# Optimization experiments

Measured on AMD Instinct MI355X. Metric: run time of the kernel, lower is better.

Reference implementation:

```python
import jax, jax.numpy as jnp
import numpy as np

B = 64        # graphs per batch
NP = 96       # nodes per graph
H = 64        # hid_size
IN_F = 32     # node feature dim
E_F = 16      # edge feature dim
DEG = 8       # avg degree
ENSEMBLE = 1


def _lin(key, fan_in, fan_out):
    return jax.random.normal(key, (fan_in, fan_out), jnp.float32) / np.float32(np.sqrt(fan_in))


def setup_inputs() -> dict:
    key = jax.random.key(0)
    ks = jax.random.split(key, 12)
    N = B * NP
    E = B * NP * DEG
    x = jax.random.normal(ks[0], (N, IN_F), jnp.float32)
    edge_attr = jax.random.normal(ks[1], (E, E_F), jnp.float32)
    # within-graph random edges (sorted per-graph blocks, like is_sorted=True)
    rng = np.random.default_rng(0)
    off = (np.arange(B) * NP)[:, None]
    src = (rng.integers(0, NP, size=(B, NP * DEG)) + off).ravel()
    dst = (rng.integers(0, NP, size=(B, NP * DEG)) + off).ravel()
    edge_index = jnp.asarray(np.stack([src, dst]), dtype=jnp.int32)
    # idx = concat of triu_indices(n, -n) per graph == ALL n^2 pairs per graph
    tri = np.triu_indices(NP, -NP)
    idx0 = jnp.asarray((tri[0][None, :] + off).ravel(), jnp.int32)  # [B*NP^2]
    idx1 = jnp.asarray((tri[1][None, :] + off).ravel(), jnp.int32)
    params = dict(
        W_atom=_lin(ks[2], IN_F, H), b_atom=jnp.zeros((H,), jnp.float32),
        W_bond=_lin(ks[3], E_F, H), b_bond=jnp.zeros((H,), jnp.float32),
        W_node=_lin(ks[4], H, H), b_node=jnp.zeros((H,), jnp.float32),
        W_edge=_lin(ks[5], H, H), b_edge=jnp.zeros((H,), jnp.float32),
        W1=_lin(ks[6], 3 * H, H), b1=jnp.zeros((H,), jnp.float32),
        W2=_lin(ks[7], H, H), b2=jnp.zeros((H,), jnp.float32),
        W3=_lin(ks[8], H, ENSEMBLE), b3=jnp.zeros((ENSEMBLE,), jnp.float32),
    )
    return dict(x=x, edge_attr=edge_attr, edge_index=edge_index,
                idx0=idx0, idx1=idx1, n=NP, **params)


def reference(x, edge_attr, edge_index, idx0, idx1, n,
              W_atom, b_atom, W_bond, b_bond, W_node, b_node,
              W_edge, b_edge, W1, b1, W2, b2, W3, b3):
    # encoders
    xh = x @ W_atom + b_atom                 # [N, H]
    eh = edge_attr @ W_bond + b_bond         # [E, H]
    emb_n = xh @ W_node + b_node             # [N, H]
    emb_e = eh @ W_edge + b_edge             # [E, H]
    # SparseTensor.to_dense() then gather at idx == scatter-add edge embeddings
    # into the per-graph dense pairwise slot (duplicates sum, missing = 0),
    # without materializing the O(N^2) adjacency.
    u, v = edge_index[0], edge_index[1]
    g = u // n
    pair_idx = g * (n * n) + (u - g * n) * n + (v - g * n)   # [E]
    P = idx0.shape[0]                         # B * n^2, idx enumerates all pairs row-major
    pair_e = jnp.zeros((P, emb_e.shape[1]), emb_e.dtype).at[pair_idx].add(emb_e)
    emb = jnp.concatenate((emb_n[idx0], emb_n[idx1], pair_e), axis=-1)  # [P, 3H]
    # MLP [3H, H, H, ensemble], plain last layer
    h = jax.nn.relu(emb @ W1 + b1)
    h = jax.nn.relu(h @ W2 + b2)
    return h @ W3 + b3                        # [P, ensemble]
```

## Files before the change

kernel.cpp:

```cpp
#include <hip/hip_runtime.h>

#define NPG 96
#define BGR 64
#define HID 64
#define INF 32
#define EF  16
#define DEG 8
#define NN  (BGR*NPG)
#define NE  (BGR*NPG*DEG)
#define EPG (NPG*DEG)
#define PPG (NPG*NPG)

typedef short bf16x8 __attribute__((ext_vector_type(8)));
typedef float f32x4  __attribute__((ext_vector_type(4)));

__device__ __forceinline__ unsigned rne2(float lo, float hi) {
    union { float f; unsigned u; } a, b; a.f = lo; b.f = hi;
    unsigned ua = a.u + 0x7FFF + ((a.u >> 16) & 1);
    unsigned ub = b.u + 0x7FFF + ((b.u >> 16) & 1);
    return (ua >> 16) | (ub & 0xFFFF0000u);
}
__device__ __forceinline__ unsigned short rne1(float x) {
    union { float f; unsigned u; } a; a.f = x;
    return (unsigned short)((a.u + 0x7FFF + ((a.u >> 16) & 1)) >> 16);
}

__global__ __launch_bounds__(256) void node_kernel(
    const float* __restrict__ x,
    const float* __restrict__ W_atom, const float* __restrict__ b_atom,
    const float* __restrict__ W_node, const float* __restrict__ b_node,
    const float* __restrict__ W1,     const float* __restrict__ b1,
    float* __restrict__ Abuf, float* __restrict__ Bbuf)
{
    __shared__ float sh[4][64];
    const int wave = threadIdx.x >> 6, lane = threadIdx.x & 63;
    const int n = __builtin_amdgcn_readfirstlane(blockIdx.x * 4 + wave);
    const float* xr = x + n * INF;

    float xh = b_atom[lane];
    #pragma unroll
    for (int k = 0; k < INF; ++k) xh += xr[k] * W_atom[k*HID + lane];
    sh[wave][lane] = xh;
    __syncthreads();

    float en = b_node[lane];
    #pragma unroll
    for (int k = 0; k < HID; ++k) en += sh[wave][k] * W_node[k*HID + lane];
    __syncthreads();
    sh[wave][lane] = en;
    __syncthreads();

    float a = b1[lane], b = 0.f;
    #pragma unroll
    for (int k = 0; k < HID; ++k) {
        const float ek = sh[wave][k];
        a += ek * W1[k*HID + lane];
        b += ek * W1[(HID + k)*HID + lane];
    }
    Abuf[n*HID + lane] = a;
    Bbuf[n*HID + lane] = b;
}

#define SBST 68
#define W2ST 72
__global__ __launch_bounds__(256) void pair_dense_kernel(
    const float* __restrict__ Abuf, const float* __restrict__ Bbuf,
    const float* __restrict__ W2,   const float* __restrict__ b2,
    const float* __restrict__ W3,   const float* __restrict__ b3,
    float* __restrict__ out)
{
    __shared__ float sB[NPG * SBST];
    __shared__ float sA[8 * 64];
    __shared__ unsigned short sW2t[64 * W2ST];
    const int t  = threadIdx.x;
    const int g  = blockIdx.x / 12;
    const int i0 = (blockIdx.x % 12) * 8;

    const float* Bg = Bbuf + g * NPG * 64;
    for (int idx = t; idx < NPG*64; idx += 256)
        sB[(idx >> 6)*SBST + (idx & 63)] = Bg[idx];
    for (int idx = t; idx < 8*64; idx += 256)
        sA[idx] = Abuf[(g*NPG + i0 + (idx >> 6))*64 + (idx & 63)];
    for (int idx = t; idx < 64*64; idx += 256) {
        const int k = idx >> 6, n = idx & 63;
        sW2t[n*W2ST + k] = rne1(W2[idx]);
    }
    __syncthreads();

    const int wave = t >> 6, lane = t & 63;
    const int col = lane & 15, q = lane >> 4;

    bf16x8 w2f[4][2];
    #pragma unroll
    for (int nt = 0; nt < 4; ++nt)
        #pragma unroll
        for (int c = 0; c < 2; ++c)
            w2f[nt][c] = *(const bf16x8*)(sW2t + (nt*16 + col)*W2ST + c*32 + q*8);

    float w3l[4], b2l[4];
    #pragma unroll
    for (int nt = 0; nt < 4; ++nt) {
        w3l[nt] = W3[nt*16 + col];
        b2l[nt] = b2[nt*16 + col];
    }
    const float b3v = b3[0];

    #pragma unroll
    for (int ii = 0; ii < 2; ++ii) {
        const int il = wave*2 + ii;
        float areg[16];
        {
            const float4* Ar = (const float4*)(sA + il*64 + q*8);
            const float4 a0 = Ar[0], a1 = Ar[1];
            const float4 a2 = Ar[8], a3 = Ar[9];
            areg[0]=a0.x; areg[1]=a0.y; areg[2]=a0.z; areg[3]=a0.w;
            areg[4]=a1.x; areg[5]=a1.y; areg[6]=a1.z; areg[7]=a1.w;
            areg[8]=a2.x; areg[9]=a2.y; areg[10]=a2.z; areg[11]=a2.w;
            areg[12]=a3.x; areg[13]=a3.y; areg[14]=a3.z; areg[15]=a3.w;
        }
        float* outr = out + g*PPG + (i0 + il)*NPG;

        for (int jc = 0; jc < 6; ++jc) {
            const int j0 = jc * 16;
            union { bf16x8 v; unsigned u[4]; } h1[2];
            const float* Brow = sB + (j0 + col)*SBST + q*8;
            #pragma unroll
            for (int c = 0; c < 2; ++c) {
                const float4 b0 = *(const float4*)(Brow + c*32);
                const float4 b1v = *(const float4*)(Brow + c*32 + 4);
                float h[8];
                h[0] = fmaxf(areg[c*8+0] + b0.x, 0.f);
                h[1] = fmaxf(areg[c*8+1] + b0.y, 0.f);
                h[2] = fmaxf(areg[c*8+2] + b0.z, 0.f);
                h[3] = fmaxf(areg[c*8+3] + b0.w, 0.f);
                h[4] = fmaxf(areg[c*8+4] + b1v.x, 0.f);
                h[5] = fmaxf(areg[c*8+5] + b1v.y, 0.f);
                h[6] = fmaxf(areg[c*8+6] + b1v.z, 0.f);
                h[7] = fmaxf(areg[c*8+7] + b1v.w, 0.f);
                #pragma unroll
                for (int p2 = 0; p2 < 4; ++p2)
                    h1[c].u[p2] = rne2(h[2*p2], h[2*p2+1]);
            }
            f32x4 acc[4];
            #pragma unroll
            for (int nt = 0; nt < 4; ++nt) {
                f32x4 z = {0.f, 0.f, 0.f, 0.f};
                z = __builtin_amdgcn_mfma_f32_16x16x32_bf16(h1[0].v, w2f[nt][0], z, 0, 0, 0);
                z = __builtin_amdgcn_mfma_f32_16x16x32_bf16(h1[1].v, w2f[nt][1], z, 0, 0, 0);
                acc[nt] = z;
            }
            float p[4];
            #pragma unroll
            for (int r = 0; r < 4; ++r) {
                float s = 0.f;
                #pragma unroll
                for (int nt = 0; nt < 4; ++nt)
                    s += fmaxf(acc[nt][r] + b2l[nt], 0.f) * w3l[nt];
                p[r] = s;
            }
            #pragma unroll
            for (int off = 1; off < 16; off <<= 1) {
                #pragma unroll
                for (int r = 0; r < 4; ++r)
                    p[r] += __shfl_xor(p[r], off, 64);
            }
            if (col == 0) {
                float4 o = make_float4(p[0]+b3v, p[1]+b3v, p[2]+b3v, p[3]+b3v);
                *(float4*)(outr + j0 + q*4) = o;
            }
        }
    }
}

__global__ __launch_bounds__(EPG) void dedup_kernel(
    const float* __restrict__ ea,  const int* __restrict__ eidx,
    const float* __restrict__ W_bond, const float* __restrict__ b_bond,
    const float* __restrict__ W_edge, const float* __restrict__ b_edge,
    const float* __restrict__ W1,
    int* __restrict__ fkey, int* __restrict__ fcnt,
    float* __restrict__ fsea, int* __restrict__ gcount,
    float* __restrict__ wec, float* __restrict__ biascg)
{
    __shared__ int   head[PPG];
    __shared__ int   nxt[EPG];
    __shared__ float sU[16*64];
    __shared__ float sbe[64];
    __shared__ int   lcnt;
    const int t = threadIdx.x;
    const int g = blockIdx.x;

    for (int idx = t; idx < PPG; idx += EPG) head[idx] = -1;
    if (t == 0) lcnt = 0;

    const int u = eidx[g*EPG + t]      - g*NPG;
    const int v = eidx[NE + g*EPG + t] - g*NPG;
    const int key = u*NPG + v;
    __syncthreads();

    nxt[t] = atomicExch(&head[key], t);
    __syncthreads();

    if (head[key] == t) {
        const float* eag = ea + (size_t)g * EPG * EF;
        float s[EF];
        #pragma unroll
        for (int q = 0; q < EF; ++q) s[q] = 0.f;
        int cnt = 0;
        for (int e = t; e != -1; e = nxt[e]) {
            ++cnt;
            const float4* p = (const float4*)(eag + e*EF);
            #pragma unroll
            for (int q4 = 0; q4 < 4; ++q4) {
                const float4 f = p[q4];
                s[q4*4+0] += f.x; s[q4*4+1] += f.y;
                s[q4*4+2] += f.z; s[q4*4+3] += f.w;
            }
        }
        const int pos  = atomicAdd(&lcnt, 1);
        const int slot = g*EPG + pos;
        fkey[slot] = key;
        fcnt[slot] = cnt;
        #pragma unroll
        for (int q = 0; q < EF; ++q) fsea[slot*EF + q] = s[q];
    }
    __syncthreads();
    if (t == 0) gcount[g] = lcnt;

    if (g == 0) {
        for (int idx = t; idx < 16*64; idx += EPG) {
            const int r = idx >> 6, c = idx & 63;
            float s = 0.f;
            for (int k = 0; k < 64; ++k) s += W_bond[r*64+k] * W_edge[k*64+c];
            sU[idx] = s;
        }
        if (t < 64) {
            float s2 = b_edge[t];
            for (int k = 0; k < 64; ++k) s2 += b_bond[k] * W_edge[k*64+t];
            sbe[t] = s2;
        }
        __syncthreads();
        for (int idx = t; idx < 16*64; idx += EPG) {
            const int r = idx >> 6, c = idx & 63;
            float s = 0.f;
            for (int k = 0; k < 64; ++k) s += sU[r*64+k] * W1[(128+k)*64+c];
            wec[idx] = s;
        }
        if (t < 64) {
            float sc = 0.f;
            for (int k = 0; k < 64; ++k) sc += sbe[k] * W1[(128+k)*64+t];
            biascg[t] = sc;
        }
    }
}

#define FIXW 16
#define FIX_BLOCKS (NE / (FIXW * 4))
__global__ __launch_bounds__(256) void fixmlp_kernel(
    const float* __restrict__ Abuf, const float* __restrict__ Bbuf,
    const int* __restrict__ fkey, const int* __restrict__ fcnt,
    const float* __restrict__ fsea, const int* __restrict__ gcount,
    const float* __restrict__ wec,  const float* __restrict__ biascg,
    const float* __restrict__ W2,   const float* __restrict__ b2,
    const float* __restrict__ W3,   const float* __restrict__ b3,
    float* __restrict__ out)
{
    __shared__ unsigned short sW2t[64 * W2ST];
    __shared__ float sWEc[16*64];
    __shared__ float sbc[64];
    const int t = threadIdx.x;

    for (int idx = t; idx < 64*64; idx += 256) {
        const int k = idx >> 6, n = idx & 63;
        sW2t[n*W2ST + k] = rne1(W2[idx]);
    }
    for (int idx = t; idx < 16*64; idx += 256) sWEc[idx] = wec[idx];
    if (t < 64) sbc[t] = biascg[t];
    __syncthreads();

    const int wave = t >> 6, lane = t & 63;
    const int col = lane & 15, q = lane >> 4;
    const int s0 = (blockIdx.x * 4 + wave) * FIXW;
    const int g  = s0 / EPG;
    const int l0 = s0 % EPG;
    const int cg = gcount[g];
    if (l0 >= cg) return;

    bf16x8 w2f[4][2];
    #pragma unroll
    for (int nt = 0; nt < 4; ++nt)
        #pragma unroll
        for (int c = 0; c < 2; ++c)
            w2f[nt][c] = *(const bf16x8*)(sW2t + (nt*16 + col)*W2ST + c*32 + q*8);

    float w3l[4], b2l[4];
    #pragma unroll
    for (int nt = 0; nt < 4; ++nt) {
        w3l[nt] = W3[nt*16 + col];
        b2l[nt] = b2[nt*16 + col];
    }
    const float b3v = b3[0];
    const int k0 = q * 8;

    union { bf16x8 v; unsigned u[4]; } h1[2];
    #pragma unroll
    for (int p2 = 0; p2 < 4; ++p2) { h1[0].u[p2] = 0; h1[1].u[p2] = 0; }

    const int s = s0 + col;
    if (l0 + col < cg) {
        const int key  = fkey[s];
        const float cf = (float)fcnt[s];
        const int ui = key / NPG, vi = key % NPG;

        float se[16];
        {
            const float4* p = (const float4*)(fsea + (size_t)s * EF);
            #pragma unroll
            for (int q4 = 0; q4 < 4; ++q4) {
                const float4 f = p[q4];
                se[q4*4+0] = f.x; se[q4*4+1] = f.y;
                se[q4*4+2] = f.z; se[q4*4+3] = f.w;
            }
        }

        float ck[16];
        #pragma unroll
        for (int kk = 0; kk < 8; ++kk) {
            ck[kk]     = cf * sbc[k0 + kk];
            ck[8 + kk] = cf * sbc[32 + k0 + kk];
        }
        #pragma unroll
        for (int qq = 0; qq < 16; ++qq) {
            const float sq = se[qq];
            const float4 w0 = *(const float4*)(sWEc + qq*64 + k0);
            const float4 w1 = *(const float4*)(sWEc + qq*64 + k0 + 4);
            const float4 w2v = *(const float4*)(sWEc + qq*64 + k0 + 32);
            const float4 w3v = *(const float4*)(sWEc + qq*64 + k0 + 36);
            ck[0]  += sq * w0.x;  ck[1]  += sq * w0.y;
            ck[2]  += sq * w0.z;  ck[3]  += sq * w0.w;
            ck[4]  += sq * w1.x;  ck[5]  += sq * w1.y;
            ck[6]  += sq * w1.z;  ck[7]  += sq * w1.w;
            ck[8]  += sq * w2v.x; ck[9]  += sq * w2v.y;
            ck[10] += sq * w2v.z; ck[11] += sq * w2v.w;
            ck[12] += sq * w3v.x; ck[13] += sq * w3v.y;
            ck[14] += sq * w3v.z; ck[15] += sq * w3v.w;
        }

        const float* Ar = Abuf + (g*NPG + ui)*64;
        const float* Br = Bbuf + (g*NPG + vi)*64;
        const float4 a0 = *(const float4*)(Ar + k0);
        const float4 a1 = *(const float4*)(Ar + k0 + 4);
        const float4 a2 = *(const float4*)(Ar + k0 + 32);
        const float4 a3 = *(const float4*)(Ar + k0 + 36);
        const float4 c0 = *(const float4*)(Br + k0);
        const float4 c1 = *(const float4*)(Br + k0 + 4);
        const float4 c2 = *(const float4*)(Br + k0 + 32);
        const float4 c3 = *(const float4*)(Br + k0 + 36);

        float h[16];
        h[0]  = fmaxf(a0.x + c0.x + ck[0],  0.f);
        h[1]  = fmaxf(a0.y + c0.y + ck[1],  0.f);
        h[2]  = fmaxf(a0.z + c0.z + ck[2],  0.f);
        h[3]  = fmaxf(a0.w + c0.w + ck[3],  0.f);
        h[4]  = fmaxf(a1.x + c1.x + ck[4],  0.f);
        h[5]  = fmaxf(a1.y + c1.y + ck[5],  0.f);
        h[6]  = fmaxf(a1.z + c1.z + ck[6],  0.f);
        h[7]  = fmaxf(a1.w + c1.w + ck[7],  0.f);
        h[8]  = fmaxf(a2.x + c2.x + ck[8],  0.f);
        h[9]  = fmaxf(a2.y + c2.y + ck[9],  0.f);
        h[10] = fmaxf(a2.z + c2.z + ck[10], 0.f);
        h[11] = fmaxf(a2.w + c2.w + ck[11], 0.f);
        h[12] = fmaxf(a3.x + c3.x + ck[12], 0.f);
        h[13] = fmaxf(a3.y + c3.y + ck[13], 0.f);
        h[14] = fmaxf(a3.z + c3.z + ck[14], 0.f);
        h[15] = fmaxf(a3.w + c3.w + ck[15], 0.f);
        #pragma unroll
        for (int p2 = 0; p2 < 4; ++p2) {
            h1[0].u[p2] = rne2(h[2*p2],     h[2*p2 + 1]);
            h1[1].u[p2] = rne2(h[8 + 2*p2], h[8 + 2*p2 + 1]);
        }
    }

    f32x4 acc[4];
    #pragma unroll
    for (int nt = 0; nt < 4; ++nt) {
        f32x4 z = {0.f, 0.f, 0.f, 0.f};
        z = __builtin_amdgcn_mfma_f32_16x16x32_bf16(h1[0].v, w2f[nt][0], z, 0, 0, 0);
        z = __builtin_amdgcn_mfma_f32_16x16x32_bf16(h1[1].v, w2f[nt][1], z, 0, 0, 0);
        acc[nt] = z;
    }

    float p[4];
    #pragma unroll
    for (int r = 0; r < 4; ++r) {
        float sum = 0.f;
        #pragma unroll
        for (int nt = 0; nt < 4; ++nt)
            sum += fmaxf(acc[nt][r] + b2l[nt], 0.f) * w3l[nt];
        p[r] = sum;
    }
    #pragma unroll
    for (int off = 1; off < 16; off <<= 1) {
        #pragma unroll
        for (int r = 0; r < 4; ++r)
            p[r] += __shfl_xor(p[r], off, 64);
    }
    if (col == 0) {
        #pragma unroll
        for (int r = 0; r < 4; ++r) {
            const int lr = q*4 + r;
            if (l0 + lr < cg) {
                const int keyr = fkey[s0 + lr];
                out[g*PPG + keyr] = p[r] + b3v;
            }
        }
    }
}

extern "C" void kernel_launch(void* const* d_in, const int* in_sizes, int n_in,
                              void* d_out, int out_size, void* d_ws, size_t ws_size,
                              hipStream_t stream)
{
    const float* x      = (const float*)d_in[0];
    const float* ea     = (const float*)d_in[1];
    const int*   eidx   = (const int*)  d_in[2];
    const float* W_atom = (const float*)d_in[6];
    const float* b_atom = (const float*)d_in[7];
    const float* W_bond = (const float*)d_in[8];
    const float* b_bond = (const float*)d_in[9];
    const float* W_node = (const float*)d_in[10];
    const float* b_node = (const float*)d_in[11];
    const float* W_edge = (const float*)d_in[12];
    const float* b_edge = (const float*)d_in[13];
    const float* W1     = (const float*)d_in[14];
    const float* b1     = (const float*)d_in[15];
    const float* W2     = (const float*)d_in[16];
    const float* b2     = (const float*)d_in[17];
    const float* W3     = (const float*)d_in[18];
    const float* b3     = (const float*)d_in[19];
    float* out = (float*)d_out;

    float* ws    = (float*)d_ws;
    float* Abuf  = ws;
    float* Bbuf  = Abuf  + NN*HID;
    float* fsea  = Bbuf  + NN*HID;
    int*   fkey  = (int*)(fsea + NE*EF);
    int*   fcnt  = fkey + NE;
    int*   gcount= fcnt + NE;
    float* wec   = (float*)(gcount + BGR);
    float* biascg= wec + 16*64;

    node_kernel<<<NN/4, 256, 0, stream>>>(x, W_atom, b_atom, W_node, b_node,
                                          W1, b1, Abuf, Bbuf);
    dedup_kernel<<<BGR, EPG, 0, stream>>>(ea, eidx, W_bond, b_bond,
                                          W_edge, b_edge, W1,
                                          fkey, fcnt, fsea, gcount,
                                          wec, biascg);
    pair_dense_kernel<<<BGR*12, 256, 0, stream>>>(Abuf, Bbuf,
                                                  W2, b2, W3, b3, out);
    fixmlp_kernel<<<FIX_BLOCKS, 256, 0, stream>>>(
        Abuf, Bbuf, fkey, fcnt, fsea, gcount, wec, biascg,
        W2, b2, W3, b3, out);
}
```

Before: 152.9 us.

## Merge four kernels into two and mask dense writes with edge bitmap

The node encoder and edge dedup kernels are fused into one prep launch that uses block-index ranges, with 12 nodes per 768-thread block. The dense pair MLP and edge-fix MLP are fused into one pair launch. A per-graph bitmap of pairs that have edges is built during dedup, and the dense path skips writing outputs for those pairs. This removes two launches and lets both pair paths run concurrently, because the fix path no longer has to overwrite dense results after them. The cost is a larger shared-memory footprint per block and per-element bitmap checks on output stores.

Result: faster. 142.4 us (-6.9%).

```diff
diff --git a/kernel.cpp b/kernel.cpp
--- a/kernel.cpp
+++ b/kernel.cpp
@@ -10,6 +10,7 @@
 #define NE  (BGR*NPG*DEG)
 #define EPG (NPG*DEG)
 #define PPG (NPG*NPG)
+#define BMW 288
 
 typedef short bf16x8 __attribute__((ext_vector_type(8)));
 typedef float f32x4  __attribute__((ext_vector_type(4)));
@@ -25,172 +26,65 @@
     return (unsigned short)((a.u + 0x7FFF + ((a.u >> 16) & 1)) >> 16);
 }
 
-__global__ __launch_bounds__(256) void node_kernel(
+__global__ __launch_bounds__(768) void prep_kernel(
     const float* __restrict__ x,
     const float* __restrict__ W_atom, const float* __restrict__ b_atom,
     const float* __restrict__ W_node, const float* __restrict__ b_node,
     const float* __restrict__ W1,     const float* __restrict__ b1,
-    float* __restrict__ Abuf, float* __restrict__ Bbuf)
-{
-    __shared__ float sh[4][64];
-    const int wave = threadIdx.x >> 6, lane = threadIdx.x & 63;
-    const int n = __builtin_amdgcn_readfirstlane(blockIdx.x * 4 + wave);
-    const float* xr = x + n * INF;
-
-    float xh = b_atom[lane];
-    #pragma unroll
-    for (int k = 0; k < INF; ++k) xh += xr[k] * W_atom[k*HID + lane];
-    sh[wave][lane] = xh;
-    __syncthreads();
-
-    float en = b_node[lane];
-    #pragma unroll
-    for (int k = 0; k < HID; ++k) en += sh[wave][k] * W_node[k*HID + lane];
-    __syncthreads();
-    sh[wave][lane] = en;
-    __syncthreads();
-
-    float a = b1[lane], b = 0.f;
-    #pragma unroll
-    for (int k = 0; k < HID; ++k) {
-        const float ek = sh[wave][k];
-        a += ek * W1[k*HID + lane];
-        b += ek * W1[(HID + k)*HID + lane];
-    }
-    Abuf[n*HID + lane] = a;
-    Bbuf[n*HID + lane] = b;
-}
-
-#define SBST 68
-#define W2ST 72
-__global__ __launch_bounds__(256) void pair_dense_kernel(
-    const float* __restrict__ Abuf, const float* __restrict__ Bbuf,
-    const float* __restrict__ W2,   const float* __restrict__ b2,
-    const float* __restrict__ W3,   const float* __restrict__ b3,
-    float* __restrict__ out)
-{
-    __shared__ float sB[NPG * SBST];
-    __shared__ float sA[8 * 64];
-    __shared__ unsigned short sW2t[64 * W2ST];
-    const int t  = threadIdx.x;
-    const int g  = blockIdx.x / 12;
-    const int i0 = (blockIdx.x % 12) * 8;
-
-    const float* Bg = Bbuf + g * NPG * 64;
-    for (int idx = t; idx < NPG*64; idx += 256)
-        sB[(idx >> 6)*SBST + (idx & 63)] = Bg[idx];
-    for (int idx = t; idx < 8*64; idx += 256)
-        sA[idx] = Abuf[(g*NPG + i0 + (idx >> 6))*64 + (idx & 63)];
-    for (int idx = t; idx < 64*64; idx += 256) {
-        const int k = idx >> 6, n = idx & 63;
-        sW2t[n*W2ST + k] = rne1(W2[idx]);
-    }
-    __syncthreads();
-
-    const int wave = t >> 6, lane = t & 63;
-    const int col = lane & 15, q = lane >> 4;
-
-    bf16x8 w2f[4][2];
-    #pragma unroll
-    for (int nt = 0; nt < 4; ++nt)
-        #pragma unroll
-        for (int c = 0; c < 2; ++c)
-            w2f[nt][c] = *(const bf16x8*)(sW2t + (nt*16 + col)*W2ST + c*32 + q*8);
-
-    float w3l[4], b2l[4];
-    #pragma unroll
-    for (int nt = 0; nt < 4; ++nt) {
-        w3l[nt] = W3[nt*16 + col];
-        b2l[nt] = b2[nt*16 + col];
-    }
-    const float b3v = b3[0];
-
-    #pragma unroll
-    for (int ii = 0; ii < 2; ++ii) {
-        const int il = wave*2 + ii;
-        float areg[16];
-        {
-            const float4* Ar = (const float4*)(sA + il*64 + q*8);
-            const float4 a0 = Ar[0], a1 = Ar[1];
-            const float4 a2 = Ar[8], a3 = Ar[9];
-            areg[0]=a0.x; areg[1]=a0.y; areg[2]=a0.z; areg[3]=a0.w;
-            areg[4]=a1.x; areg[5]=a1.y; areg[6]=a1.z; areg[7]=a1.w;
-            areg[8]=a2.x; areg[9]=a2.y; areg[10]=a2.z; areg[11]=a2.w;
-            areg[12]=a3.x; areg[13]=a3.y; areg[14]=a3.z; areg[15]=a3.w;
-        }
-        float* outr = out + g*PPG + (i0 + il)*NPG;
-
-        for (int jc = 0; jc < 6; ++jc) {
-            const int j0 = jc * 16;
-            union { bf16x8 v; unsigned u[4]; } h1[2];
-            const float* Brow = sB + (j0 + col)*SBST + q*8;
-            #pragma unroll
-            for (int c = 0; c < 2; ++c) {
-                const float4 b0 = *(const float4*)(Brow + c*32);
-                const float4 b1v = *(const float4*)(Brow + c*32 + 4);
-                float h[8];
-                h[0] = fmaxf(areg[c*8+0] + b0.x, 0.f);
-                h[1] = fmaxf(areg[c*8+1] + b0.y, 0.f);
-                h[2] = fmaxf(areg[c*8+2] + b0.z, 0.f);
-                h[3] = fmaxf(areg[c*8+3] + b0.w, 0.f);
-                h[4] = fmaxf(areg[c*8+4] + b1v.x, 0.f);
-                h[5] = fmaxf(areg[c*8+5] + b1v.y, 0.f);
-                h[6] = fmaxf(areg[c*8+6] + b1v.z, 0.f);
-                h[7] = fmaxf(areg[c*8+7] + b1v.w, 0.f);
-                #pragma unroll
-                for (int p2 = 0; p2 < 4; ++p2)
-                    h1[c].u[p2] = rne2(h[2*p2], h[2*p2+1]);
-            }
-            f32x4 acc[4];
-            #pragma unroll
-            for (int nt = 0; nt < 4; ++nt) {
-                f32x4 z = {0.f, 0.f, 0.f, 0.f};
-                z = __builtin_amdgcn_mfma_f32_16x16x32_bf16(h1[0].v, w2f[nt][0], z, 0, 0, 0);
-                z = __builtin_amdgcn_mfma_f32_16x16x32_bf16(h1[1].v, w2f[nt][1], z, 0, 0, 0);
-                acc[nt] = z;
-            }
-            float p[4];
-            #pragma unroll
-            for (int r = 0; r < 4; ++r) {
-                float s = 0.f;
-                #pragma unroll
-                for (int nt = 0; nt < 4; ++nt)
-                    s += fmaxf(acc[nt][r] + b2l[nt], 0.f) * w3l[nt];
-                p[r] = s;
-            }
-            #pragma unroll
-            for (int off = 1; off < 16; off <<= 1) {
-                #pragma unroll
-                for (int r = 0; r < 4; ++r)
-                    p[r] += __shfl_xor(p[r], off, 64);
-            }
-            if (col == 0) {
-                float4 o = make_float4(p[0]+b3v, p[1]+b3v, p[2]+b3v, p[3]+b3v);
-                *(float4*)(outr + j0 + q*4) = o;
-            }
-        }
-    }
-}
-
-__global__ __launch_bounds__(EPG) void dedup_kernel(
-    const float* __restrict__ ea,  const int* __restrict__ eidx,
+    const float* __restrict__ ea,     const int* __restrict__ eidx,
     const float* __restrict__ W_bond, const float* __restrict__ b_bond,
     const float* __restrict__ W_edge, const float* __restrict__ b_edge,
-    const float* __restrict__ W1,
+    float* __restrict__ Abuf, float* __restrict__ Bbuf,
     int* __restrict__ fkey, int* __restrict__ fcnt,
     float* __restrict__ fsea, int* __restrict__ gcount,
-    float* __restrict__ wec, float* __restrict__ biascg)
+    float* __restrict__ wec, float* __restrict__ biascg,
+    unsigned* __restrict__ gbm)
 {
-    __shared__ int   head[PPG];
-    __shared__ int   nxt[EPG];
-    __shared__ float sU[16*64];
-    __shared__ float sbe[64];
-    __shared__ int   lcnt;
+    __shared__ __align__(16) char smem[45504];
     const int t = threadIdx.x;
+
+    if (blockIdx.x >= 64) {
+        float* sh = (float*)smem;
+        const int wave = t >> 6, lane = t & 63;
+        const int n = __builtin_amdgcn_readfirstlane((blockIdx.x - 64)*12 + wave);
+        const float* xr = x + n * INF;
+
+        float xh = b_atom[lane];
+        #pragma unroll
+        for (int k = 0; k < INF; ++k) xh += xr[k] * W_atom[k*HID + lane];
+        sh[wave*64 + lane] = xh;
+        __syncthreads();
+
+        float en = b_node[lane];
+        #pragma unroll
+        for (int k = 0; k < HID; ++k) en += sh[wave*64 + k] * W_node[k*HID + lane];
+        __syncthreads();
+        sh[wave*64 + lane] = en;
+        __syncthreads();
+
+        float a = b1[lane], b = 0.f;
+        #pragma unroll
+        for (int k = 0; k < HID; ++k) {
+            const float ek = sh[wave*64 + k];
+            a += ek * W1[k*HID + lane];
+            b += ek * W1[(HID + k)*HID + lane];
+        }
+        Abuf[n*HID + lane] = a;
+        Bbuf[n*HID + lane] = b;
+        return;
+    }
+
+    int*      head = (int*)smem;
+    int*      nxt  = (int*)(smem + 36864);
+    float*    sU   = (float*)(smem + 36864 + 3072);
+    float*    sbe  = (float*)(smem + 36864 + 3072 + 4096);
+    unsigned* bm   = (unsigned*)(smem + 36864+3072+4096+256);
+    int*      lcnt = (int*)(smem + 36864+3072+4096+256+1152);
     const int g = blockIdx.x;
 
     for (int idx = t; idx < PPG; idx += EPG) head[idx] = -1;
-    if (t == 0) lcnt = 0;
+    for (int idx = t; idx < BMW; idx += EPG) bm[idx] = 0u;
+    if (t == 0) *lcnt = 0;
 
     const int u = eidx[g*EPG + t]      - g*NPG;
     const int v = eidx[NE + g*EPG + t] - g*NPG;
@@ -216,7 +110,8 @@
                 s[q4*4+2] += f.z; s[q4*4+3] += f.w;
             }
         }
-        const int pos  = atomicAdd(&lcnt, 1);
+        atomicOr(&bm[key >> 5], 1u << (key & 31));
+        const int pos  = atomicAdd(lcnt, 1);
         const int slot = g*EPG + pos;
         fkey[slot] = key;
         fcnt[slot] = cnt;
@@ -224,7 +119,8 @@
         for (int q = 0; q < EF; ++q) fsea[slot*EF + q] = s[q];
     }
     __syncthreads();
-    if (t == 0) gcount[g] = lcnt;
+    for (int idx = t; idx < BMW; idx += EPG) gbm[g*BMW + idx] = bm[idx];
+    if (t == 0) gcount[g] = *lcnt;
 
     if (g == 0) {
         for (int idx = t; idx < 16*64; idx += EPG) {
@@ -253,21 +149,134 @@
     }
 }
 
+#define SBST 68
+#define W2ST 72
 #define FIXW 16
-#define FIX_BLOCKS (NE / (FIXW * 4))
-__global__ __launch_bounds__(256) void fixmlp_kernel(
+__global__ __launch_bounds__(256) void pair_kernel(
     const float* __restrict__ Abuf, const float* __restrict__ Bbuf,
     const int* __restrict__ fkey, const int* __restrict__ fcnt,
     const float* __restrict__ fsea, const int* __restrict__ gcount,
     const float* __restrict__ wec,  const float* __restrict__ biascg,
+    const unsigned* __restrict__ gbm,
     const float* __restrict__ W2,   const float* __restrict__ b2,
     const float* __restrict__ W3,   const float* __restrict__ b3,
     float* __restrict__ out)
 {
-    __shared__ unsigned short sW2t[64 * W2ST];
-    __shared__ float sWEc[16*64];
-    __shared__ float sbc[64];
+    __shared__ __align__(16) char smem[37504];
     const int t = threadIdx.x;
+    const int wave = t >> 6, lane = t & 63;
+    const int col = lane & 15, q = lane >> 4;
+    const float b3v = b3[0];
+
+    if (blockIdx.x < 768) {
+        float*          sB   = (float*)smem;
+        float*          sA   = (float*)(smem + 26112);
+        unsigned short* sW2t = (unsigned short*)(smem + 28160);
+        unsigned*       sBM  = (unsigned*)(smem + 28160 + 9216);
+        const int g  = blockIdx.x / 12;
+        const int i0 = (blockIdx.x % 12) * 8;
+
+        const float* Bg = Bbuf + g * NPG * 64;
+        for (int idx = t; idx < NPG*64; idx += 256)
+            sB[(idx >> 6)*SBST + (idx & 63)] = Bg[idx];
+        for (int idx = t; idx < 8*64; idx += 256)
+            sA[idx] = Abuf[(g*NPG + i0 + (idx >> 6))*64 + (idx & 63)];
+        for (int idx = t; idx < 64*64; idx += 256) {
+            const int k = idx >> 6, n = idx & 63;
+            sW2t[n*W2ST + k] = rne1(W2[idx]);
+        }
+        if (t < 24) sBM[t] = gbm[g*BMW + i0*3 + t];
+        __syncthreads();
+
+        bf16x8 w2f[4][2];
+        #pragma unroll
+        for (int nt = 0; nt < 4; ++nt)
+            #pragma unroll
+            for (int c = 0; c < 2; ++c)
+                w2f[nt][c] = *(const bf16x8*)(sW2t + (nt*16 + col)*W2ST + c*32 + q*8);
+
+        float w3l[4], b2l[4];
+        #pragma unroll
+        for (int nt = 0; nt < 4; ++nt) {
+            w3l[nt] = W3[nt*16 + col];
+            b2l[nt] = b2[nt*16 + col];
+        }
+
+        #pragma unroll
+        for (int ii = 0; ii < 2; ++ii) {
+            const int il = wave*2 + ii;
+            float areg[16];
+            {
+                const float4* Ar = (const float4*)(sA + il*64 + q*8);
+                const float4 a0 = Ar[0], a1 = Ar[1];
+                const float4 a2 = Ar[8], a3 = Ar[9];
+                areg[0]=a0.x; areg[1]=a0.y; areg[2]=a0.z; areg[3]=a0.w;
+                areg[4]=a1.x; areg[5]=a1.y; areg[6]=a1.z; areg[7]=a1.w;
+                areg[8]=a2.x; areg[9]=a2.y; areg[10]=a2.z; areg[11]=a2.w;
+                areg[12]=a3.x; areg[13]=a3.y; areg[14]=a3.z; areg[15]=a3.w;
+            }
+            float* outr = out + g*PPG + (i0 + il)*NPG;
+
+            for (int jc = 0; jc < 6; ++jc) {
+                const int j0 = jc * 16;
+                union { bf16x8 v; unsigned u[4]; } h1[2];
+                const float* Brow = sB + (j0 + col)*SBST + q*8;
+                #pragma unroll
+                for (int c = 0; c < 2; ++c) {
+                    const float4 b0 = *(const float4*)(Brow + c*32);
+                    const float4 b1v = *(const float4*)(Brow + c*32 + 4);
+                    float h[8];
+                    h[0] = fmaxf(areg[c*8+0] + b0.x, 0.f);
+                    h[1] = fmaxf(areg[c*8+1] + b0.y, 0.f);
+                    h[2] = fmaxf(areg[c*8+2] + b0.z, 0.f);
+                    h[3] = fmaxf(areg[c*8+3] + b0.w, 0.f);
+                    h[4] = fmaxf(areg[c*8+4] + b1v.x, 0.f);
+                    h[5] = fmaxf(areg[c*8+5] + b1v.y, 0.f);
+                    h[6] = fmaxf(areg[c*8+6] + b1v.z, 0.f);
+                    h[7] = fmaxf(areg[c*8+7] + b1v.w, 0.f);
+                    #pragma unroll
+                    for (int p2 = 0; p2 < 4; ++p2)
+                        h1[c].u[p2] = rne2(h[2*p2], h[2*p2+1]);
+                }
+                f32x4 acc[4];
+                #pragma unroll
+                for (int nt = 0; nt < 4; ++nt) {
+                    f32x4 z = {0.f, 0.f, 0.f, 0.f};
+                    z = __builtin_amdgcn_mfma_f32_16x16x32_bf16(h1[0].v, w2f[nt][0], z, 0, 0, 0);
+                    z = __builtin_amdgcn_mfma_f32_16x16x32_bf16(h1[1].v, w2f[nt][1], z, 0, 0, 0);
+                    acc[nt] = z;
+                }
+                float p[4];
+                #pragma unroll
+                for (int r = 0; r < 4; ++r) {
+                    float s = 0.f;
+                    #pragma unroll
+                    for (int nt = 0; nt < 4; ++nt)
+                        s += fmaxf(acc[nt][r] + b2l[nt], 0.f) * w3l[nt];
+                    p[r] = s;
+                }
+                #pragma unroll
+                for (int off = 1; off < 16; off <<= 1) {
+                    #pragma unroll
+                    for (int r = 0; r < 4; ++r)
+                        p[r] += __shfl_xor(p[r], off, 64);
+                }
+                if (col == 0) {
+                    #pragma unroll
+                    for (int r = 0; r < 4; ++r) {
+                        const int j = j0 + q*4 + r;
+                        if (!((sBM[il*3 + (j >> 5)] >> (j & 31)) & 1u))
+                            outr[j] = p[r] + b3v;
+                    }
+                }
+            }
+        }
+        return;
+    }
+
+    unsigned short* sW2t = (unsigned short*)smem;
+    float*          sWEc = (float*)(smem + 9216);
+    float*          sbc  = (float*)(smem + 9216 + 4096);
 
     for (int idx = t; idx < 64*64; idx += 256) {
         const int k = idx >> 6, n = idx & 63;
@@ -277,9 +286,8 @@
     if (t < 64) sbc[t] = biascg[t];
     __syncthreads();
 
-    const int wave = t >> 6, lane = t & 63;
-    const int col = lane & 15, q = lane >> 4;
-    const int s0 = (blockIdx.x * 4 + wave) * FIXW;
+    const int fb = blockIdx.x - 768;
+    const int s0 = (fb * 4 + wave) * FIXW;
     const int g  = s0 / EPG;
     const int l0 = s0 % EPG;
     const int cg = gcount[g];
@@ -298,7 +306,6 @@
         w3l[nt] = W3[nt*16 + col];
         b2l[nt] = b2[nt*16 + col];
     }
-    const float b3v = b3[0];
     const int k0 = q * 8;
 
     union { bf16x8 v; unsigned u[4]; } h1[2];
@@ -448,16 +455,13 @@
     int*   gcount= fcnt + NE;
     float* wec   = (float*)(gcount + BGR);
     float* biascg= wec + 16*64;
-
-    node_kernel<<<NN/4, 256, 0, stream>>>(x, W_atom, b_atom, W_node, b_node,
-                                          W1, b1, Abuf, Bbuf);
-    dedup_kernel<<<BGR, EPG, 0, stream>>>(ea, eidx, W_bond, b_bond,
-                                          W_edge, b_edge, W1,
-                                          fkey, fcnt, fsea, gcount,
-                                          wec, biascg);
-    pair_dense_kernel<<<BGR*12, 256, 0, stream>>>(Abuf, Bbuf,
-                                                  W2, b2, W3, b3, out);
-    fixmlp_kernel<<<FIX_BLOCKS, 256, 0, stream>>>(
-        Abuf, Bbuf, fkey, fcnt, fsea, gcount, wec, biascg,
+    unsigned* gbm= (unsigned*)(biascg + 64);
+
+    prep_kernel<<<64 + NN/12, 768, 0, stream>>>(
+        x, W_atom, b_atom, W_node, b_node, W1, b1,
+        ea, eidx, W_bond, b_bond, W_edge, b_edge,
+        Abuf, Bbuf, fkey, fcnt, fsea, gcount, wec, biascg, gbm);
+    pair_kernel<<<768 + NE/(FIXW*4), 256, 0, stream>>>(
+        Abuf, Bbuf, fkey, fcnt, fsea, gcount, wec, biascg, gbm,
         W2, b2, W3, b3, out);
 }
```
